# Performance work log

Hardware: AMD Instinct MI355X
Metric: run time of the kernel (lower is better)

The kernel has to match this reference:

```python
import jax, jax.numpy as jnp
import numpy as np

WS = 8  # window size
NUM_HEAD = 8
DIM_HEAD = 64


def _rel_pos_index(ws):
    coords = np.stack(np.meshgrid(np.arange(ws), np.arange(ws), indexing='ij'))  # (2, ws, ws)
    cf = coords.reshape(2, -1)                       # (2, A)
    rel = cf[:, :, None] - cf[:, None, :]            # (2, A, A)
    rel = rel.transpose(1, 2, 0).astype(np.int32)    # (A, A, 2)
    rel[:, :, 0] += ws - 1
    rel[:, :, 1] += ws - 1
    rel[:, :, 0] *= 2 * ws - 1
    return jnp.asarray(rel.sum(-1))                  # (A, A) int32


def setup_inputs() -> dict:
    key = jax.random.key(0)
    k0, k1, k2 = jax.random.split(key, 3)
    B, Hh, dh, H, W = 4, NUM_HEAD, DIM_HEAD, 128, 128
    C = Hh * dh
    qkv = jax.random.normal(k0, (B, Hh, 3 * dh, H, W), dtype=jnp.float32)
    logit_scale = jnp.log(10.0) * jnp.ones((Hh, 1, 1), dtype=jnp.float32)
    rpb_table = 0.02 * jax.random.normal(k1, ((2 * WS - 1) * (2 * WS - 1), Hh), dtype=jnp.float32)
    proj_w = 0.02 * jax.random.normal(k2, (C, C), dtype=jnp.float32)
    proj_b = jnp.zeros((C,), dtype=jnp.float32)
    rel_index = _rel_pos_index(WS)
    return {"qkv": qkv, "logit_scale": logit_scale, "rpb_table": rpb_table,
            "proj_w": proj_w, "proj_b": proj_b, "rel_index": rel_index}


def reference(qkv, logit_scale, rpb_table, proj_w, proj_b, rel_index):
    B, Hh, C3, H, W = qkv.shape
    ws = WS
    dh = C3 // 3
    A = ws * ws
    nH, nW = H // ws, W // ws
    # window partition: (B, Hh, C3, H, W) -> (B*nH*nW, Hh, A, C3)
    x = qkv.reshape(B, Hh, C3, nH, ws, nW, ws)
    x = x.transpose(0, 3, 5, 1, 4, 6, 2).reshape(-1, Hh, A, C3)
    q, k, v = jnp.split(x, 3, axis=-1)
    # cosine attention: L2-normalize q, k (eps matches F.normalize)
    q = q / jnp.maximum(jnp.linalg.norm(q, axis=-1, keepdims=True), 1e-12)
    k = k / jnp.maximum(jnp.linalg.norm(k, axis=-1, keepdims=True), 1e-12)
    attn = jnp.einsum('whqd,whkd->whqk', q, k)
    scale = jnp.exp(jnp.minimum(logit_scale, jnp.log(100.0)))  # clamp max=log(1/0.01)
    attn = attn * scale[None]
    # relative position bias: (A,A,Hh) -> (1,Hh,A,A)
    bias = rpb_table[rel_index.reshape(-1)].reshape(A, A, Hh).transpose(2, 0, 1)
    attn = jax.nn.softmax(attn + bias[None], axis=-1)
    out = jnp.einsum('whqk,whkd->whqd', attn, v)  # (B*nH*nW, Hh, A, dh)
    # window unpartition -> (B, Hh*dh, H, W)
    out = out.reshape(B, nH, nW, Hh, ws, ws, dh)
    out = out.transpose(0, 3, 6, 1, 4, 2, 5).reshape(B, Hh * dh, H, W)
    # 1x1 conv projection
    out = jnp.einsum('oc,bchw->bohw', proj_w, out) + proj_b[None, :, None, None]
    return out
```

## Files before the change

kernel.cpp:

```cpp
#include <hip/hip_runtime.h>

typedef _Float16 f16;
typedef f16 f16x2 __attribute__((ext_vector_type(2)));
typedef f16 f16x4 __attribute__((ext_vector_type(4)));
typedef f16 f16x8 __attribute__((ext_vector_type(8)));
typedef float floatx4 __attribute__((ext_vector_type(4)));

#define LDS_AS(p) ((__attribute__((address_space(3))) unsigned int*)(p))
#define GLB_AS(p) ((const __attribute__((address_space(1))) unsigned int*)(p))

__device__ __forceinline__ void gload16(const void* g, void* l) {
  __builtin_amdgcn_global_load_lds(GLB_AS(g), LDS_AS(l), 16, 0, 0);
}

__global__ __launch_bounds__(256) void wconv_kernel(const float* __restrict__ w,
                                                    f16* __restrict__ wh) {
  const int i = (blockIdx.x * 256 + threadIdx.x) * 4;
  const float4 v = *(const float4*)(w + i);
  f16x4 o;
  o.x = (f16)v.x; o.y = (f16)v.y; o.z = (f16)v.z; o.w = (f16)v.w;
  *(f16x4*)(wh + i) = o;
}

__global__ __launch_bounds__(256) void attn_kernel(
    const float* __restrict__ qkv, const float* __restrict__ logit_scale,
    const float* __restrict__ rpb, const int* __restrict__ rel_index,
    f16* __restrict__ X) {
  __shared__ f16 qs[64 * 72];
  __shared__ f16 ks[64 * 72];
  __shared__ f16 vs[64 * 72];
  __shared__ f16 ps[64 * 72];

  const int bid = blockIdx.x;
  const int h   = bid & 7;
  const int win = bid >> 3;
  const int wx  = win & 15;
  const int wy  = (win >> 4) & 15;
  const int b   = win >> 8;

  const int tid  = threadIdx.x;
  const int wave = tid >> 6;
  const int lane = tid & 63;

  {
    const int c    = tid >> 2;
    const int quad = tid & 3;
    const int xh   = quad & 1;
    const int tyb  = quad >> 1;
    const size_t base = (size_t)((b * 8 + h) * 192) * 16384 +
                        (size_t)(wy * 8) * 128 + wx * 8 + xh * 4;
    const float* qp = qkv + base + (size_t)c * 16384;
    const float* kp = qkv + base + (size_t)(64 + c) * 16384;
    const float* vp = qkv + base + (size_t)(128 + c) * 16384;
#pragma unroll
    for (int j = 0; j < 4; j++) {
      const int ty = 2 * j + tyb;
      const int t0 = ty * 8 + xh * 4;
      const float4 qv = *(const float4*)(qp + ty * 128);
      const float4 kv = *(const float4*)(kp + ty * 128);
      const float4 vv = *(const float4*)(vp + ty * 128);
      qs[(t0 + 0) * 72 + c] = (f16)qv.x;
      qs[(t0 + 1) * 72 + c] = (f16)qv.y;
      qs[(t0 + 2) * 72 + c] = (f16)qv.z;
      qs[(t0 + 3) * 72 + c] = (f16)qv.w;
      ks[(t0 + 0) * 72 + c] = (f16)kv.x;
      ks[(t0 + 1) * 72 + c] = (f16)kv.y;
      ks[(t0 + 2) * 72 + c] = (f16)kv.z;
      ks[(t0 + 3) * 72 + c] = (f16)kv.w;
      vs[c * 72 + t0 + 0] = (f16)vv.x;
      vs[c * 72 + t0 + 1] = (f16)vv.y;
      vs[c * 72 + t0 + 2] = (f16)vv.z;
      vs[c * 72 + t0 + 3] = (f16)vv.w;
    }
  }
  __syncthreads();

  {
    const int token = (tid & 127) >> 1;
    const int half  = tid & 1;
    f16* rowp = ((tid < 128) ? qs : ks) + token * 72 + half * 32;
    f16x8 d[4];
    float ssq = 0.f;
#pragma unroll
    for (int i = 0; i < 4; i++) {
      d[i] = *(const f16x8*)(rowp + i * 8);
#pragma unroll
      for (int e = 0; e < 8; e++) {
        const float f = (float)d[i][e];
        ssq += f * f;
      }
    }
    ssq += __shfl_xor(ssq, 1);
    const float rs = 1.0f / fmaxf(sqrtf(ssq), 1e-12f);
#pragma unroll
    for (int i = 0; i < 4; i++) {
#pragma unroll
      for (int e = 0; e < 8; e++) d[i][e] = (f16)((float)d[i][e] * rs);
      *(f16x8*)(rowp + i * 8) = d[i];
    }
  }
  __syncthreads();

  const int fr = lane & 15;
  const int g  = lane >> 4;
  const int m0 = wave * 16;
  const float scale = __expf(fminf(logit_scale[h], 4.60517019f));

  floatx4 acc[4];
  {
    const f16x8 a0 = *(const f16x8*)(qs + (m0 + fr) * 72 + g * 8);
    const f16x8 a1 = *(const f16x8*)(qs + (m0 + fr) * 72 + 32 + g * 8);
#pragma unroll
    for (int nt = 0; nt < 4; nt++) {
      const f16x8 b0 = *(const f16x8*)(ks + (nt * 16 + fr) * 72 + g * 8);
      const f16x8 b1 = *(const f16x8*)(ks + (nt * 16 + fr) * 72 + 32 + g * 8);
      floatx4 z = {0.f, 0.f, 0.f, 0.f};
      z = __builtin_amdgcn_mfma_f32_16x16x32_f16(a0, b0, z, 0, 0, 0);
      z = __builtin_amdgcn_mfma_f32_16x16x32_f16(a1, b1, z, 0, 0, 0);
      acc[nt] = z;
    }
  }

#pragma unroll
  for (int r = 0; r < 4; r++) {
    const int m = m0 + g * 4 + r;
    float v0[4];
    float mx = -1e30f;
#pragma unroll
    for (int nt = 0; nt < 4; nt++) {
      const int n = nt * 16 + fr;
      const float val = acc[nt][r] * scale + rpb[rel_index[m * 64 + n] * 8 + h];
      v0[nt] = val;
      mx = fmaxf(mx, val);
    }
    mx = fmaxf(mx, __shfl_xor(mx, 1));
    mx = fmaxf(mx, __shfl_xor(mx, 2));
    mx = fmaxf(mx, __shfl_xor(mx, 4));
    mx = fmaxf(mx, __shfl_xor(mx, 8));
    float s = 0.f;
#pragma unroll
    for (int nt = 0; nt < 4; nt++) {
      v0[nt] = __expf(v0[nt] - mx);
      s += v0[nt];
    }
    s += __shfl_xor(s, 1);
    s += __shfl_xor(s, 2);
    s += __shfl_xor(s, 4);
    s += __shfl_xor(s, 8);
    const float rinv = 1.0f / s;
#pragma unroll
    for (int nt = 0; nt < 4; nt++)
      ps[m * 72 + nt * 16 + fr] = (f16)(v0[nt] * rinv);
  }

  floatx4 oacc[4];
  {
    const f16x8 pa0 = *(const f16x8*)(ps + (m0 + fr) * 72 + g * 8);
    const f16x8 pa1 = *(const f16x8*)(ps + (m0 + fr) * 72 + 32 + g * 8);
#pragma unroll
    for (int dt = 0; dt < 4; dt++) {
      const f16x8 vb0 = *(const f16x8*)(vs + (dt * 16 + fr) * 72 + g * 8);
      const f16x8 vb1 = *(const f16x8*)(vs + (dt * 16 + fr) * 72 + 32 + g * 8);
      floatx4 z = {0.f, 0.f, 0.f, 0.f};
      z = __builtin_amdgcn_mfma_f32_16x16x32_f16(pa0, vb0, z, 0, 0, 0);
      z = __builtin_amdgcn_mfma_f32_16x16x32_f16(pa1, vb1, z, 0, 0, 0);
      oacc[dt] = z;
    }
  }

#pragma unroll
  for (int r = 0; r < 4; r++) {
    const int m = m0 + g * 4 + r;
    const int ty = m >> 3, tx = m & 7;
    const size_t npix = (size_t)(b * 128 + wy * 8 + ty) * 128 + wx * 8 + tx;
    f16* xp = X + npix * 512 + h * 64;
#pragma unroll
    for (int dt = 0; dt < 4; dt++) xp[dt * 16 + fr] = (f16)oacc[dt][r];
  }
}

__global__ __launch_bounds__(256) void proj_kernel(
    const f16* __restrict__ Wh, const f16* __restrict__ X,
    const float* __restrict__ bias, float* __restrict__ out) {
  __shared__ f16 As[128 * 64];
  __shared__ f16 Bs[128 * 64];

  const int tid  = threadIdx.x;
  const int lane = tid & 63;
  const int wave = tid >> 6;
  const int o0 = (blockIdx.x & 3) * 128;
  const int p0 = (blockIdx.x >> 2) * 128;

  const int fr = lane & 15, g = lane >> 4;
  const int wr = wave >> 1, wc = wave & 1;

  floatx4 acc[4][4] = {};

  const f16* gA[4];
  const f16* gB[4];
#pragma unroll
  for (int j = 0; j < 4; j++) {
    const int slot = j * 256 + tid;
    const int row  = slot >> 3;
    const int c8   = (tid & 7) ^ (row & 7);
    gA[j] = Wh + (size_t)(o0 + row) * 512 + c8 * 8;
    gB[j] = X  + (size_t)(p0 + row) * 512 + c8 * 8;
  }

  for (int kc = 0; kc < 512; kc += 64) {
#pragma unroll
    for (int j = 0; j < 4; j++) {
      gload16(gA[j] + kc, As + (j * 256 + tid) * 8);
      gload16(gB[j] + kc, Bs + (j * 256 + tid) * 8);
    }
    __syncthreads();
#pragma unroll
    for (int kk = 0; kk < 2; kk++) {
      f16x8 af[4], bfr[4];
#pragma unroll
      for (int mt = 0; mt < 4; mt++) {
        const int row = wr * 64 + mt * 16 + fr;
        af[mt] = *(const f16x8*)(As + row * 64 + (((kk * 4 + g) ^ (row & 7)) * 8));
      }
#pragma unroll
      for (int nt = 0; nt < 4; nt++) {
        const int row = wc * 64 + nt * 16 + fr;
        bfr[nt] = *(const f16x8*)(Bs + row * 64 + (((kk * 4 + g) ^ (row & 7)) * 8));
      }
#pragma unroll
      for (int mt = 0; mt < 4; mt++)
#pragma unroll
        for (int nt = 0; nt < 4; nt++)
          acc[mt][nt] = __builtin_amdgcn_mfma_f32_16x16x32_f16(af[mt], bfr[nt],
                                                               acc[mt][nt], 0, 0, 0);
    }
    __syncthreads();
  }

  const int bidx = p0 >> 14;
  const int rem0 = p0 & 16383;
#pragma unroll
  for (int mt = 0; mt < 4; mt++) {
#pragma unroll
    for (int r = 0; r < 4; r++) {
      const int o = o0 + wr * 64 + mt * 16 + g * 4 + r;
      const float bv = bias[o];
      float* op = out + ((size_t)(bidx * 512 + o) << 14) + rem0 + wc * 64;
#pragma unroll
      for (int nt = 0; nt < 4; nt++) op[nt * 16 + fr] = acc[mt][nt][r] + bv;
    }
  }
}

extern "C" void kernel_launch(void* const* d_in, const int* in_sizes, int n_in,
                              void* d_out, int out_size, void* d_ws, size_t ws_size,
                              hipStream_t stream) {
  const float* qkv         = (const float*)d_in[0];
  const float* logit_scale = (const float*)d_in[1];
  const float* rpb         = (const float*)d_in[2];
  const float* proj_w      = (const float*)d_in[3];
  const float* proj_b      = (const float*)d_in[4];
  const int*   rel_index   = (const int*)d_in[5];
  float* out = (float*)d_out;

  f16* Wh = (f16*)d_ws;
  f16* X  = (f16*)((char*)d_ws + (512 * 512 * 2));

  hipLaunchKernelGGL(wconv_kernel, dim3(256), dim3(256), 0, stream, proj_w, Wh);
  hipLaunchKernelGGL(attn_kernel, dim3(8192), dim3(256), 0, stream,
                     qkv, logit_scale, rpb, rel_index, X);
  hipLaunchKernelGGL(proj_kernel, dim3(2048), dim3(256), 0, stream,
                     Wh, X, proj_b, out);
}
```

Baseline: 645.3 us.

## Precompute gathered bias table, vectorize qkv staging and output stores, reuse LDS

Adds a prologue in the weight-conversion kernel that materializes the relative position bias per head in an MFMA-friendly order, so the attention kernel reads one float4 instead of a double indirect gather. Reworks qkv staging so each thread loads four channels by four tokens and writes packed f16x4 to LDS. It also aliases the probability buffer onto the q buffer and stages the output through LDS to emit 16-byte coalesced stores to X. The cost is an extra workspace buffer, an extra barrier, and less per-load coalescing along channels.

```diff
diff --git a/kernel.cpp b/kernel.cpp
--- a/kernel.cpp
+++ b/kernel.cpp
@@ -13,23 +13,34 @@
   __builtin_amdgcn_global_load_lds(GLB_AS(g), LDS_AS(l), 16, 0, 0);
 }
 
-__global__ __launch_bounds__(256) void wconv_kernel(const float* __restrict__ w,
-                                                    f16* __restrict__ wh) {
-  const int i = (blockIdx.x * 256 + threadIdx.x) * 4;
-  const float4 v = *(const float4*)(w + i);
-  f16x4 o;
-  o.x = (f16)v.x; o.y = (f16)v.y; o.z = (f16)v.z; o.w = (f16)v.w;
-  *(f16x4*)(wh + i) = o;
+__global__ __launch_bounds__(256) void wconv_kernel(
+    const float* __restrict__ w, f16* __restrict__ wh,
+    const float* __restrict__ rpb, const int* __restrict__ rel_index,
+    float* __restrict__ biasT) {
+  if (blockIdx.x < 256) {
+    const int i = (blockIdx.x * 256 + threadIdx.x) * 4;
+    const float4 v = *(const float4*)(w + i);
+    f16x4 o;
+    o.x = (f16)v.x; o.y = (f16)v.y; o.z = (f16)v.z; o.w = (f16)v.w;
+    *(f16x4*)(wh + i) = o;
+  } else {
+    const int o  = (blockIdx.x - 256) * 256 + threadIdx.x;
+    const int fr = o & 15;
+    const int m  = (o >> 4) & 63;
+    const int h  = o >> 10;
+#pragma unroll
+    for (int nt = 0; nt < 4; nt++)
+      biasT[o * 4 + nt] = rpb[rel_index[m * 64 + nt * 16 + fr] * 8 + h];
+  }
 }
 
 __global__ __launch_bounds__(256) void attn_kernel(
     const float* __restrict__ qkv, const float* __restrict__ logit_scale,
-    const float* __restrict__ rpb, const int* __restrict__ rel_index,
-    f16* __restrict__ X) {
+    const float* __restrict__ biasT, f16* __restrict__ X) {
   __shared__ f16 qs[64 * 72];
   __shared__ f16 ks[64 * 72];
   __shared__ f16 vs[64 * 72];
-  __shared__ f16 ps[64 * 72];
+  f16* const ps = qs;
 
   const int bid = blockIdx.x;
   const int h   = bid & 7;
@@ -43,34 +54,37 @@
   const int lane = tid & 63;
 
   {
-    const int c    = tid >> 2;
-    const int quad = tid & 3;
-    const int xh   = quad & 1;
-    const int tyb  = quad >> 1;
+    const int c0 = (tid >> 4) * 4;
+    const int tq = tid & 15;
+    const int t0 = tq * 4;
+    const int ty = t0 >> 3;
+    const int xh = (t0 >> 2) & 1;
     const size_t base = (size_t)((b * 8 + h) * 192) * 16384 +
-                        (size_t)(wy * 8) * 128 + wx * 8 + xh * 4;
-    const float* qp = qkv + base + (size_t)c * 16384;
-    const float* kp = qkv + base + (size_t)(64 + c) * 16384;
-    const float* vp = qkv + base + (size_t)(128 + c) * 16384;
+                        (size_t)(wy * 8 + ty) * 128 + wx * 8 + xh * 4;
+    const float* gp = qkv + base;
+    floatx4 q4[4], k4[4], v4[4];
+#pragma unroll
+    for (int cc = 0; cc < 4; cc++) {
+      q4[cc] = *(const floatx4*)(gp + (size_t)(c0 + cc) * 16384);
+      k4[cc] = *(const floatx4*)(gp + (size_t)(64 + c0 + cc) * 16384);
+      v4[cc] = *(const floatx4*)(gp + (size_t)(128 + c0 + cc) * 16384);
+    }
 #pragma unroll
     for (int j = 0; j < 4; j++) {
-      const int ty = 2 * j + tyb;
-      const int t0 = ty * 8 + xh * 4;
-      const float4 qv = *(const float4*)(qp + ty * 128);
-      const float4 kv = *(const float4*)(kp + ty * 128);
-      const float4 vv = *(const float4*)(vp + ty * 128);
-      qs[(t0 + 0) * 72 + c] = (f16)qv.x;
-      qs[(t0 + 1) * 72 + c] = (f16)qv.y;
-      qs[(t0 + 2) * 72 + c] = (f16)qv.z;
-      qs[(t0 + 3) * 72 + c] = (f16)qv.w;
-      ks[(t0 + 0) * 72 + c] = (f16)kv.x;
-      ks[(t0 + 1) * 72 + c] = (f16)kv.y;
-      ks[(t0 + 2) * 72 + c] = (f16)kv.z;
-      ks[(t0 + 3) * 72 + c] = (f16)kv.w;
-      vs[c * 72 + t0 + 0] = (f16)vv.x;
-      vs[c * 72 + t0 + 1] = (f16)vv.y;
-      vs[c * 72 + t0 + 2] = (f16)vv.z;
-      vs[c * 72 + t0 + 3] = (f16)vv.w;
+      f16x4 qh, kh;
+      qh.x = (f16)q4[0][j]; qh.y = (f16)q4[1][j];
+      qh.z = (f16)q4[2][j]; qh.w = (f16)q4[3][j];
+      kh.x = (f16)k4[0][j]; kh.y = (f16)k4[1][j];
+      kh.z = (f16)k4[2][j]; kh.w = (f16)k4[3][j];
+      *(f16x4*)(qs + (t0 + j) * 72 + c0) = qh;
+      *(f16x4*)(ks + (t0 + j) * 72 + c0) = kh;
+    }
+#pragma unroll
+    for (int cc = 0; cc < 4; cc++) {
+      f16x4 vh;
+      vh.x = (f16)v4[cc][0]; vh.y = (f16)v4[cc][1];
+      vh.z = (f16)v4[cc][2]; vh.w = (f16)v4[cc][3];
+      *(f16x4*)(vs + (c0 + cc) * 72 + t0) = vh;
     }
   }
   __syncthreads();
@@ -105,6 +119,7 @@
   const int g  = lane >> 4;
   const int m0 = wave * 16;
   const float scale = __expf(fminf(logit_scale[h], 4.60517019f));
+  const float* biasH = biasT + h * 4096;
 
   floatx4 acc[4];
   {
@@ -124,12 +139,12 @@
 #pragma unroll
   for (int r = 0; r < 4; r++) {
     const int m = m0 + g * 4 + r;
+    const floatx4 bv = *(const floatx4*)(biasH + m * 64 + fr * 4);
     float v0[4];
     float mx = -1e30f;
 #pragma unroll
     for (int nt = 0; nt < 4; nt++) {
-      const int n = nt * 16 + fr;
-      const float val = acc[nt][r] * scale + rpb[rel_index[m * 64 + n] * 8 + h];
+      const float val = acc[nt][r] * scale + bv[nt];
       v0[nt] = val;
       mx = fmaxf(mx, val);
     }
@@ -171,11 +186,20 @@
 #pragma unroll
   for (int r = 0; r < 4; r++) {
     const int m = m0 + g * 4 + r;
-    const int ty = m >> 3, tx = m & 7;
+#pragma unroll
+    for (int dt = 0; dt < 4; dt++)
+      ps[m * 72 + dt * 16 + fr] = (f16)oacc[dt][r];
+  }
+  __syncthreads();
+
+  {
+    const int t  = tid >> 2;
+    const int ci = (tid & 3) * 16;
+    const int ty = t >> 3, tx = t & 7;
     const size_t npix = (size_t)(b * 128 + wy * 8 + ty) * 128 + wx * 8 + tx;
-    f16* xp = X + npix * 512 + h * 64;
-#pragma unroll
-    for (int dt = 0; dt < 4; dt++) xp[dt * 16 + fr] = (f16)oacc[dt][r];
+    f16* xp = X + npix * 512 + h * 64 + ci;
+    *(f16x8*)(xp)     = *(const f16x8*)(ps + t * 72 + ci);
+    *(f16x8*)(xp + 8) = *(const f16x8*)(ps + t * 72 + ci + 8);
   }
 }
 
@@ -263,12 +287,14 @@
   const int*   rel_index   = (const int*)d_in[5];
   float* out = (float*)d_out;
 
-  f16* Wh = (f16*)d_ws;
-  f16* X  = (f16*)((char*)d_ws + (512 * 512 * 2));
-
-  hipLaunchKernelGGL(wconv_kernel, dim3(256), dim3(256), 0, stream, proj_w, Wh);
+  f16*   Wh    = (f16*)d_ws;
+  f16*   X     = (f16*)((char*)d_ws + (512 * 512 * 2));
+  float* biasT = (float*)((char*)d_ws + (512 * 512 * 2) + (65536 * 512 * 2));
+
+  hipLaunchKernelGGL(wconv_kernel, dim3(288), dim3(256), 0, stream,
+                     proj_w, Wh, rpb, rel_index, biasT);
   hipLaunchKernelGGL(attn_kernel, dim3(8192), dim3(256), 0, stream,
-                     qkv, logit_scale, rpb, rel_index, X);
+                     qkv, logit_scale, biasT, X);
   hipLaunchKernelGGL(proj_kernel, dim3(2048), dim3(256), 0, stream,
                      Wh, X, proj_b, out);
 }
```

Measured after the change: 638.1 us. No clear change (-1.1%).
